# Optimization experiments

Measured on AMD Instinct MI355X. Metric: run time of the kernel, lower is better.

Reference implementation:

```python
import jax, jax.numpy as jnp
import numpy as np

B, S, NB, ORDER, D = 256, 50, 8, 2, 128
N_ITEMS, N_RELS = 100000, 200
STDV = 1.0 / float(np.sqrt(D))  # reset_parameters: uniform(-1/sqrt(hidden), 1/sqrt(hidden))


def setup_inputs() -> dict:
    key = jax.random.key(0)
    ks = jax.random.split(key, 24)
    u = lambda k, shape: jax.random.uniform(k, shape, jnp.float32, -STDV, STDV)
    return {
        'h_iids': jax.random.randint(ks[0], (B, S), 1, N_ITEMS),
        'a_iids': jax.random.randint(ks[1], (B,), 0, N_ITEMS),
        'adj_entity': jax.random.randint(ks[2], (N_ITEMS, NB), 0, N_ITEMS),
        'adj_relation': jax.random.randint(ks[3], (N_ITEMS, NB), 0, N_RELS),
        'item_emb': u(ks[4], (N_ITEMS, D)),
        'rel_emb': u(ks[5], (N_RELS, D)),
        'Wa': u(ks[6], (D, 1)), 'ba': u(ks[7], (1,)),          # linear_attention
        'Wt': u(ks[8], (D, D)), 'bt': u(ks[9], (D,)),          # linear_attention_transform
        'Wih': u(ks[10], (D, 3 * D)), 'Whh': u(ks[11], (D, 3 * D)),  # GRU (1 layer)
        'bih': u(ks[12], (3 * D,)), 'bhh': u(ks[13], (3 * D,)),
        'W1': u(ks[14], (D, D)), 'b1': u(ks[15], (D,)),        # linear_one
        'W2': u(ks[16], (D, D)), 'b2': u(ks[17], (D,)),        # linear_two
        'W3': u(ks[18], (D, 1)),                               # linear_three (no bias)
        'Wtr': u(ks[19], (2 * D, D)), 'btr': u(ks[20], (D,)),  # linear_transform
    }


def _forward(h_iids, adj_entity, adj_relation, item_emb, rel_emb,
             Wa, ba, Wt, bt, Wih, Whh, bih, bhh,
             W1, b1, W2, b2, W3, Wtr, btr):
    # ---- get_neighbors: multi-hop KG neighbor expansion ----
    entities = [h_iids]           # level 0: [B, S]
    relations = []
    for i in range(ORDER):
        e = entities[i]
        entities.append(adj_entity[e].reshape(B, -1))    # [B, S*NB^(i+1)]
        relations.append(adj_relation[e].reshape(B, -1))
    ent_embs = [item_emb[e] for e in entities]           # gathers
    rel_embs = [rel_emb[r] for r in relations]
    # ---- high_order_aggregate: attention-weighted neighbor aggregation ----
    neib = ent_embs[ORDER]                                # [B, S*NB^ORDER, D]
    for i in range(ORDER):
        self_e = ent_embs[ORDER - i - 1]                  # [B, M, D]
        rel = rel_embs[ORDER - i - 1].reshape(B, -1, NB, D)
        nb4 = neib.reshape(rel.shape)                     # [B, M, NB, D]
        att = (self_e[:, :, None, :] * rel * nb4) @ Wa + ba   # [B, M, NB, 1]
        alpha = jax.nn.softmax(att, axis=2)
        agg = jnp.sum(nb4 * alpha, axis=2)                # [B, M, D]
        neib = (self_e + agg) @ Wt + bt                   # aggregate='sum' branch
    item_embs = neib                                      # [B, S, D] (sigmoid in src is dead code)
    # ---- GRU, 1 layer, batch_first ----
    def step(h, x):
        gi = x @ Wih + bih
        gh = h @ Whh + bhh
        ir, iz, inn = jnp.split(gi, 3, axis=-1)
        hr, hz, hn = jnp.split(gh, 3, axis=-1)
        r = jax.nn.sigmoid(ir + hr)
        z = jax.nn.sigmoid(iz + hz)
        n = jnp.tanh(inn + r * hn)
        h2 = (1.0 - z) * n + z * h
        return h2, h2
    h0 = jnp.zeros((B, D), jnp.float32)
    _, outs = jax.lax.scan(step, h0, jnp.swapaxes(item_embs, 0, 1))
    output = jnp.swapaxes(outs, 0, 1)                     # [B, S, D]
    # ---- attention pooling over sequence ----
    last_idx = jnp.clip(jnp.sum(h_iids != 0, axis=1) - 1, 0, S - 1)
    local_ht = output[jnp.arange(B), last_idx]            # [B, D]
    q1 = (local_ht @ W1 + b1)[:, None, :]
    q2 = output @ W2 + b2
    al = jax.nn.sigmoid(q1 + q2) @ W3                     # [B, S, 1]
    global_ht = jnp.sum(al * output, axis=1)
    ght = jnp.concatenate([local_ht, global_ht], axis=1) @ Wtr + btr
    logits = jax.nn.relu(ght @ item_emb.T)                # [B, n_items]
    return logits


def reference(h_iids, a_iids, adj_entity, adj_relation, item_emb, rel_emb,
              Wa, ba, Wt, bt, Wih, Whh, bih, bhh,
              W1, b1, W2, b2, W3, Wtr, btr):
    # a_iids is accepted by forward() but unused (matches the torch source).
    return _forward(h_iids, adj_entity, adj_relation, item_emb, rel_emb,
                    Wa, ba, Wt, bt, Wih, Whh, bih, bhh,
                    W1, b1, W2, b2, W3, Wtr, btr)
```

## Files before the change

### kernel.cpp

```cpp
#include <hip/hip_runtime.h>
#include <hip/hip_bf16.h>
#include <math.h>

#define NB_B 256
#define NB_S 50
#define NB_NB 8
#define NB_D 128
#define NB_NITEMS 100000

#define C_RZ (-1.442695041f)
#define C_N (2.885390082f)

typedef __attribute__((ext_vector_type(8))) short short8;
typedef __attribute__((ext_vector_type(4))) float f32x4;
typedef unsigned int uint;
typedef unsigned short ushort;

__device__ __forceinline__ ushort f2bf(float f) {
  union { float f; uint u; } v;
  v.f = f;
  return (ushort)((v.u + 0x7fffu + ((v.u >> 16) & 1u)) >> 16);
}
__device__ __forceinline__ uint packbf(float a, float b) {
  return (uint)f2bf(a) | ((uint)f2bf(b) << 16);
}
__device__ __forceinline__ float bflo(uint u) {
  union { uint u; float f; } v; v.u = u << 16; return v.f;
}
__device__ __forceinline__ float bfhi(uint u) {
  union { uint u; float f; } v; v.u = u & 0xffff0000u; return v.f;
}
__device__ __forceinline__ float bf2f(ushort u) {
  union { uint u; float f; } v; v.u = (uint)u << 16; return v.f;
}
__device__ __forceinline__ void unpack8(uint4 u, float* f) {
  f[0] = bflo(u.x); f[1] = bfhi(u.x);
  f[2] = bflo(u.y); f[3] = bfhi(u.y);
  f[4] = bflo(u.z); f[5] = bfhi(u.z);
  f[6] = bflo(u.w); f[7] = bfhi(u.w);
}

__device__ __forceinline__ void castf_body(const float* __restrict__ src,
                                           uint* __restrict__ dst, int i, int n8) {
  if (i >= n8) return;
  float4 a = ((const float4*)src)[2 * i];
  float4 b = ((const float4*)src)[2 * i + 1];
  uint4 o;
  o.x = packbf(a.x, a.y);
  o.y = packbf(a.z, a.w);
  o.z = packbf(b.x, b.y);
  o.w = packbf(b.z, b.w);
  ((uint4*)dst)[i] = o;
}
template <int CO, bool SCALED>
__device__ __forceinline__ void castT_body(const float* __restrict__ W,
                                           ushort* __restrict__ WT, int idx) {
  if (idx >= 128 * CO) return;
  int n = idx >> 7, k = idx & 127;
  float v = W[(size_t)k * CO + n];
  if (SCALED) v *= (n < 256 ? C_RZ : C_N);
  WT[idx] = f2bf(v);
}
__global__ __launch_bounds__(256) void prep_kernel(
    const float* __restrict__ item_emb, const float* __restrict__ rel_emb,
    const float* __restrict__ Wt, const float* __restrict__ Wih,
    const float* __restrict__ Whh, const float* __restrict__ W2,
    const float* __restrict__ bih, const float* __restrict__ bhh,
    uint* __restrict__ EMB_BF, uint* __restrict__ REL_BF,
    ushort* __restrict__ WtT, ushort* __restrict__ WihT,
    ushort* __restrict__ WhhT, ushort* __restrict__ W2T,
    float* __restrict__ GIBIAS) {
  int bx = blockIdx.x, tid = threadIdx.x;
  if (bx < 6250) {
    castf_body(item_emb, EMB_BF, bx * 256 + tid, 1600000);
  } else if (bx < 6263) {
    castf_body(rel_emb, REL_BF, (bx - 6250) * 256 + tid, 3200);
  } else if (bx < 6327) {
    castT_body<128, false>(Wt, WtT, (bx - 6263) * 256 + tid);
  } else if (bx < 6519) {
    castT_body<384, true>(Wih, WihT, (bx - 6327) * 256 + tid);
  } else if (bx < 6711) {
    castT_body<384, true>(Whh, WhhT, (bx - 6519) * 256 + tid);
  } else if (bx < 6775) {
    castT_body<128, false>(W2, W2T, (bx - 6711) * 256 + tid);
  } else {
    int idx = (bx - 6775) * 256 + tid;
    if (idx < 384) {
      float s = (idx < 256) ? C_RZ : C_N;
      GIBIAS[idx] = s * bih[idx] + (idx < 256 ? s * bhh[idx] : 0.f);
    }
  }
}

__device__ __forceinline__ uint4 hop_pair4(
    int e_self, int q, int p, const int* __restrict__ adj_e,
    const int* __restrict__ adj_r, const uint* __restrict__ embB,
    const uint* __restrict__ relB, const uint* __restrict__ neibB,
    const float* __restrict__ Wa, float* __restrict__ alds) {
  uint4 us = ((const uint4*)(embB + (size_t)e_self * 64))[q];
  float s[8], wa[8], sw[8];
  unpack8(us, s);
  *(float4*)&wa[0] = ((const float4*)Wa)[q * 2];
  *(float4*)&wa[4] = ((const float4*)Wa)[q * 2 + 1];
#pragma unroll
  for (int d = 0; d < 8; d++) sw[d] = s[d] * wa[d];

  int4 ra = ((const int4*)(adj_r + (size_t)e_self * 8))[0];
  int4 rb = ((const int4*)(adj_r + (size_t)e_self * 8))[1];
  int rk[8] = {ra.x, ra.y, ra.z, ra.w, rb.x, rb.y, rb.z, rb.w};

  uint4 nbp[8];
  if (neibB == nullptr) {
    int4 ea = ((const int4*)(adj_e + (size_t)e_self * 8))[0];
    int4 eb = ((const int4*)(adj_e + (size_t)e_self * 8))[1];
    int e2[8] = {ea.x, ea.y, ea.z, ea.w, eb.x, eb.y, eb.z, eb.w};
#pragma unroll
    for (int k = 0; k < 8; k++)
      nbp[k] = ((const uint4*)(embB + (size_t)e2[k] * 64))[q];
  } else {
#pragma unroll
    for (int k = 0; k < 8; k++)
      nbp[k] = ((const uint4*)(neibB + ((size_t)p * 8 + k) * 64))[q];
  }

  float t[8];
#pragma unroll
  for (int k = 0; k < 8; k++) {
    uint4 ur = ((const uint4*)(relB + (size_t)rk[k] * 64))[q];
    float rr[8], nb[8];
    unpack8(ur, rr);
    unpack8(nbp[k], nb);
    float tt = 0.f;
#pragma unroll
    for (int d = 0; d < 8; d++) tt = fmaf(sw[d] * rr[d], nb[d], tt);
    t[k] = tt;
  }

  bool b0 = (q & 1), b1 = (q & 2), b2 = (q & 4);
  float a4[4];
#pragma unroll
  for (int i = 0; i < 4; i++) {
    float send = b0 ? t[i] : t[4 + i];
    float recv = __shfl_xor(send, 1);
    a4[i] = (b0 ? t[4 + i] : t[i]) + recv;
  }
  float a2[2];
#pragma unroll
  for (int i = 0; i < 2; i++) {
    float send = b1 ? a4[i] : a4[2 + i];
    float recv = __shfl_xor(send, 2);
    a2[i] = (b1 ? a4[2 + i] : a4[i]) + recv;
  }
  float send1 = b2 ? a2[0] : a2[1];
  float recv1 = __shfl_xor(send1, 4);
  float c = (b2 ? a2[1] : a2[0]) + recv1;
  c += __shfl_xor(c, 8);

  float e = __expf(c);
  float den = e;
  den += __shfl_xor(den, 1);
  den += __shfl_xor(den, 2);
  den += __shfl_xor(den, 4);
  float alpha = e * __builtin_amdgcn_rcpf(den);

  int kstar = (q & 1) * 4 + (q & 2) + ((q & 4) >> 2);
  if (q < 8) alds[kstar] = alpha;
  asm volatile("s_waitcnt lgkmcnt(0)" ::: "memory");
  float a8[8];
  *(float4*)&a8[0] = ((const float4*)alds)[0];
  *(float4*)&a8[4] = ((const float4*)alds)[1];

  float x[8];
#pragma unroll
  for (int d = 0; d < 8; d++) x[d] = s[d];
#pragma unroll
  for (int k = 0; k < 8; k++) {
    float nb[8];
    unpack8(nbp[k], nb);
#pragma unroll
    for (int d = 0; d < 8; d++) x[d] = fmaf(a8[k], nb[d], x[d]);
  }
  uint4 o;
  o.x = packbf(x[0], x[1]);
  o.y = packbf(x[2], x[3]);
  o.z = packbf(x[4], x[5]);
  o.w = packbf(x[6], x[7]);
  return o;
}

__global__ __launch_bounds__(256) void hoplin_kernel(
    const int* __restrict__ h_iids, const int* __restrict__ adj_e,
    const int* __restrict__ adj_r, const uint* __restrict__ embB,
    const uint* __restrict__ relB, const float* __restrict__ Wa,
    const ushort* __restrict__ WtT, const float* __restrict__ bt,
    ushort* __restrict__ NEIB) {
  __shared__ ushort X0s[32 * 128];
  __shared__ float als[16][8];
  const int bx = blockIdx.x;
  const int wv = threadIdx.x >> 6, ln = threadIdx.x & 63;
  const int g = ln >> 4, q = ln & 15;
  float* alds = als[wv * 4 + g];

#pragma unroll
  for (int it = 0; it < 2; it++) {
    int lrow = wv * 8 + it * 4 + g;
    int p = bx * 32 + lrow;
    int b = p / (NB_S * NB_NB);
    int m = p % (NB_S * NB_NB);
    int s = m >> 3, jj = m & 7;
    int h = h_iids[b * NB_S + s];
    int e_self = adj_e[h * NB_NB + jj];
    uint4 o = hop_pair4(e_self, q, p, adj_e, adj_r, embB, relB, nullptr, Wa, alds);
    int byte = (lrow * 256 + q * 16) ^ ((lrow & 7) << 4);
    *(uint4*)((char*)X0s + byte) = o;
  }
  __syncthreads();

  const int lr = ln & 15, lg = ln >> 4;
  short8 afr[2][4];
#pragma unroll
  for (int mf = 0; mf < 2; mf++)
#pragma unroll
    for (int kf = 0; kf < 4; kf++) {
      int row = mf * 16 + lr;
      int byte = (row * 256 + lg * 16 + kf * 64) ^ ((row & 7) << 4);
      afr[mf][kf] = *(const short8*)((const char*)X0s + byte);
    }
  f32x4 acc[2][2] = {};
#pragma unroll
  for (int nf = 0; nf < 2; nf++) {
    int n = (wv * 2 + nf) * 16 + lr;
    const ushort* bb = WtT + (size_t)n * 128 + lg * 8;
#pragma unroll
    for (int kf = 0; kf < 4; kf++) {
      short8 b = *(const short8*)(bb + kf * 32);
#pragma unroll
      for (int mf = 0; mf < 2; mf++)
        acc[mf][nf] = __builtin_amdgcn_mfma_f32_16x16x32_bf16(afr[mf][kf], b,
                                                              acc[mf][nf], 0, 0, 0);
    }
  }
#pragma unroll
  for (int mf = 0; mf < 2; mf++)
#pragma unroll
    for (int nf = 0; nf < 2; nf++) {
      int n = (wv * 2 + nf) * 16 + lr;
      float bv = bt[n];
#pragma unroll
      for (int r = 0; r < 4; r++) {
        int mg = bx * 32 + mf * 16 + lg * 4 + r;
        NEIB[(size_t)mg * 128 + n] = f2bf(acc[mf][nf][r] + bv);
      }
    }
}

__global__ __launch_bounds__(256) void hop1_kernel(
    const int* __restrict__ h_iids, const int* __restrict__ adj_e,
    const int* __restrict__ adj_r, const uint* __restrict__ embB,
    const uint* __restrict__ relB, const uint* __restrict__ neibB,
    const float* __restrict__ Wa, uint* __restrict__ Xout) {
  __shared__ float als[16][8];
  const int wv = threadIdx.x >> 6, ln = threadIdx.x & 63;
  const int g = ln >> 4, q = ln & 15;
  int p = blockIdx.x * 16 + wv * 4 + g;
  int e_self = h_iids[p];
  uint4 o = hop_pair4(e_self, q, p, adj_e, adj_r, embB, relB, neibB, Wa,
                      als[wv * 4 + g]);
  ((uint4*)(Xout + (size_t)p * 64))[q] = o;
}

template <int CO, int MPW, bool OUT_BF>
__global__ __launch_bounds__(256) void linm_kernel(
    const ushort* __restrict__ Xbf, const ushort* __restrict__ WT,
    const float* __restrict__ bias, float* __restrict__ Yf,
    ushort* __restrict__ Yb, int nrows) {
  constexpr int NF = CO / 16;
  constexpr int MF = MPW / 16;
  int wave = (int)(blockIdx.x * 4 + (threadIdx.x >> 6));
  int ln = threadIdx.x & 63;
  int m0 = __builtin_amdgcn_readfirstlane(wave) * MPW;
  if (m0 >= nrows) return;
  int lr = ln & 15, lg = ln >> 4;

  short8 afr[MF][4];
#pragma unroll
  for (int mf = 0; mf < MF; mf++) {
    const ushort* ab = Xbf + (size_t)(m0 + mf * 16 + lr) * 128 + lg * 8;
#pragma unroll
    for (int kf = 0; kf < 4; kf++) afr[mf][kf] = *(const short8*)(ab + kf * 32);
  }
  f32x4 acc[MF][NF] = {};
#pragma unroll
  for (int nf = 0; nf < NF; nf++) {
    const ushort* bb = WT + (size_t)(nf * 16 + lr) * 128 + lg * 8;
#pragma unroll
    for (int kf = 0; kf < 4; kf++) {
      short8 b = *(const short8*)(bb + kf * 32);
#pragma unroll
      for (int mf = 0; mf < MF; mf++)
        acc[mf][nf] = __builtin_amdgcn_mfma_f32_16x16x32_bf16(afr[mf][kf], b,
                                                              acc[mf][nf], 0, 0, 0);
    }
  }
#pragma unroll
  for (int mf = 0; mf < MF; mf++)
#pragma unroll
    for (int nf = 0; nf < NF; nf++) {
      int n = nf * 16 + lr;
      float bv = bias[n];
#pragma unroll
      for (int r = 0; r < 4; r++) {
        int m = m0 + mf * 16 + lg * 4 + r;
        float val = acc[mf][nf][r] + bv;
        if (OUT_BF)
          Yb[(size_t)m * CO + n] = f2bf(val);
        else
          Yf[(size_t)m * CO + n] = val;
      }
    }
}

__global__ __launch_bounds__(512) void gru_mfma_kernel(
    const float* __restrict__ GI, const ushort* __restrict__ WhhT_bf,
    const float* __restrict__ bhh, ushort* __restrict__ OUTB) {
  const int b0 = blockIdx.x * 16;
  const int tid = threadIdx.x;
  const int w = tid >> 6, ln = tid & 63;
  const int lr = ln & 15, lg = ln >> 4;
  const int j = w * 16 + lr;

  __shared__ ushort hA[16 * 128];
  __shared__ ushort hB[16 * 128];

  short8 bfr[3][4];
#pragma unroll
  for (int g = 0; g < 3; g++) {
    const ushort* bb = WhhT_bf + (size_t)(g * 128 + j) * 128 + lg * 8;
#pragma unroll
    for (int kf = 0; kf < 4; kf++) bfr[g][kf] = *(const short8*)(bb + kf * 32);
  }
  const float bhn = C_N * bhh[256 + j];

  float h_reg[4] = {0.f, 0.f, 0.f, 0.f};

  {
    uint* hz = (uint*)hA;
#pragma unroll
    for (int i = tid; i < 1024; i += 512) hz[i] = 0;
  }
  __syncthreads();

  float girA[4][3], girB[4][3], girC[4][3], girD[4][3];
#pragma unroll
  for (int r = 0; r < 4; r++) {
    const float* g0 = GI + ((size_t)(b0 + lg * 4 + r) * NB_S + 0) * 384 + j;
    girA[r][0] = g0[0]; girA[r][1] = g0[128]; girA[r][2] = g0[256];
    const float* g1 = GI + ((size_t)(b0 + lg * 4 + r) * NB_S + 1) * 384 + j;
    girB[r][0] = g1[0]; girB[r][1] = g1[128]; girB[r][2] = g1[256];
    const float* g2 = GI + ((size_t)(b0 + lg * 4 + r) * NB_S + 2) * 384 + j;
    girC[r][0] = g2[0]; girC[r][1] = g2[128]; girC[r][2] = g2[256];
  }

  auto STEP = [&](int t, ushort* hRead, ushort* hWrite, float (&cur)[4][3],
                  float (&pre3)[4][3]) {
    if (t + 3 < NB_S) {
#pragma unroll
      for (int r = 0; r < 4; r++) {
        const float* g = GI + ((size_t)(b0 + lg * 4 + r) * NB_S + (t + 3)) * 384 + j;
        pre3[r][0] = g[0]; pre3[r][1] = g[128]; pre3[r][2] = g[256];
      }
    }
    __builtin_amdgcn_sched_barrier(0);
    short8 afr[4];
#pragma unroll
    for (int kf = 0; kf < 4; kf++) {
      int byte = (lr * 256 + kf * 64 + lg * 16) ^ ((lr & 7) << 4);
      afr[kf] = *(const short8*)((const char*)hRead + byte);
    }
    f32x4 acc[3] = {};
#pragma unroll
    for (int g = 0; g < 3; g++)
#pragma unroll
      for (int kf = 0; kf < 4; kf++)
        acc[g] = __builtin_amdgcn_mfma_f32_16x16x32_bf16(afr[kf], bfr[g][kf],
                                                         acc[g], 0, 0, 0);
#pragma unroll
    for (int r = 0; r < 4; r++) {
      int b = lg * 4 + r;
      float rg = __builtin_amdgcn_rcpf(
          1.f + __builtin_amdgcn_exp2f(cur[r][0] + acc[0][r]));
      float ze = __builtin_amdgcn_exp2f(cur[r][1] + acc[1][r]);
      float xp = cur[r][2] + rg * (bhn + acc[2][r]);
      float e2 = __builtin_amdgcn_exp2f(xp);
      float n = 1.f - 2.f * __builtin_amdgcn_rcpf(e2 + 1.f);
      float h2 = n + (h_reg[r] - n) * __builtin_amdgcn_rcpf(1.f + ze);
      h_reg[r] = h2;
      ushort hb = f2bf(h2);
      OUTB[((size_t)(b0 + b) * NB_S + t) * 128 + j] = hb;
      int byte = (b * 256 + j * 2) ^ ((b & 7) << 4);
      *(ushort*)((char*)hWrite + byte) = hb;
    }
    asm volatile("s_waitcnt lgkmcnt(0)" ::: "memory");
    __builtin_amdgcn_s_barrier();
  };

  for (int g4 = 0; g4 < 12; g4++) {
    int t = g4 * 4;
    STEP(t + 0, hA, hB, girA, girD);
    STEP(t + 1, hB, hA, girB, girA);
    STEP(t + 2, hA, hB, girC, girB);
    STEP(t + 3, hB, hA, girD, girC);
  }
  STEP(48, hA, hB, girA, girD);
  STEP(49, hB, hA, girB, girA);
}

__global__ __launch_bounds__(256) void pool_kernel(
    const int* __restrict__ h_iids, const ushort* __restrict__ OUTB,
    const float* __restrict__ W1, const float* __restrict__ b1,
    const ushort* __restrict__ W2T, const float* __restrict__ b2,
    const float* __restrict__ W3, const float* __restrict__ Wtr,
    const float* __restrict__ btr, ushort* __restrict__ GHT_bf) {
  const int b = blockIdx.x, tid = threadIdx.x;
  __shared__ float lh[128];
  __shared__ float q1[128];
  __shared__ float al[64];
  __shared__ float cat[256];

  if (tid < 128) {
    int cnt = 0;
    for (int s = 0; s < NB_S; s++) cnt += (h_iids[b * NB_S + s] != 0);
    int li = min(max(cnt - 1, 0), NB_S - 1);
    lh[tid] = bf2f(OUTB[((size_t)b * NB_S + li) * 128 + tid]);
  }
  __syncthreads();
  if (tid < 128) {
    float acc = b1[tid];
    for (int d = 0; d < 128; d++) acc += lh[d] * W1[(size_t)d * 128 + tid];
    q1[tid] = acc;
  }
  __syncthreads();

  {
    const int wv = tid >> 6, ln = tid & 63, lr = ln & 15, lg = ln >> 4;
    const int s0 = wv * 16;
    short8 zz = {0, 0, 0, 0, 0, 0, 0, 0};
    short8 afr[4];
    int srow = s0 + lr;
#pragma unroll
    for (int kf = 0; kf < 4; kf++)
      afr[kf] = (srow < NB_S)
                    ? *(const short8*)(OUTB + ((size_t)b * NB_S + srow) * 128 +
                                       lg * 8 + kf * 32)
                    : zz;
    float part[4] = {0.f, 0.f, 0.f, 0.f};
#pragma unroll
    for (int nf = 0; nf < 8; nf++) {
      const ushort* bb = W2T + (size_t)(nf * 16 + lr) * 128 + lg * 8;
      f32x4 acc = {};
#pragma unroll
      for (int kf = 0; kf < 4; kf++) {
        short8 bv = *(const short8*)(bb + kf * 32);
        acc = __builtin_amdgcn_mfma_f32_16x16x32_bf16(afr[kf], bv, acc, 0, 0, 0);
      }
      int c = nf * 16 + lr;
      float qc = q1[c] + b2[c];
      float w3 = W3[c];
#pragma unroll
      for (int r = 0; r < 4; r++)
        part[r] += w3 / (1.f + __expf(-(qc + acc[r])));
    }
#pragma unroll
    for (int r = 0; r < 4; r++) {
#pragma unroll
      for (int off = 1; off < 16; off <<= 1) part[r] += __shfl_xor(part[r], off);
      int s = s0 + lg * 4 + r;
      if (lr == 0 && s < NB_S) al[s] = part[r];
    }
  }
  __syncthreads();

  if (tid < 128) {
    float g = 0.f;
    for (int s = 0; s < NB_S; s++)
      g += al[s] * bf2f(OUTB[((size_t)b * NB_S + s) * 128 + tid]);
    cat[tid] = lh[tid];
    cat[128 + tid] = g;
  }
  __syncthreads();
  if (tid < 128) {
    float acc = btr[tid];
    for (int dd = 0; dd < 256; dd++) acc += cat[dd] * Wtr[(size_t)dd * 128 + tid];
    GHT_bf[b * 128 + tid] = f2bf(acc);
  }
}

__global__ __launch_bounds__(256) void logits_mfma_kernel(
    const ushort* __restrict__ GHT_bf, const ushort* __restrict__ embB,
    float* __restrict__ out) {
  int wave = (int)(blockIdx.x * 4 + (threadIdx.x >> 6));
  int ln = threadIdx.x & 63;
  int n0 = __builtin_amdgcn_readfirstlane(wave) * 32;
  if (n0 >= NB_NITEMS) return;
  int lr = ln & 15, lg = ln >> 4;

  short8 bfr[2][4];
#pragma unroll
  for (int nf = 0; nf < 2; nf++) {
    const ushort* base = embB + (size_t)(n0 + nf * 16 + lr) * 128 + lg * 8;
#pragma unroll
    for (int kf = 0; kf < 4; kf++) bfr[nf][kf] = *(const short8*)(base + kf * 32);
  }

  f32x4 acc[16][2] = {};
#pragma unroll
  for (int mg = 0; mg < 4; mg++) {
    short8 afr[4][4];
#pragma unroll
    for (int mf = 0; mf < 4; mf++) {
      const ushort* ab = GHT_bf + (size_t)((mg * 4 + mf) * 16 + lr) * 128 + lg * 8;
#pragma unroll
      for (int kf = 0; kf < 4; kf++) afr[mf][kf] = *(const short8*)(ab + kf * 32);
    }
#pragma unroll
    for (int mf = 0; mf < 4; mf++)
#pragma unroll
      for (int nf = 0; nf < 2; nf++)
#pragma unroll
        for (int kf = 0; kf < 4; kf++)
          acc[mg * 4 + mf][nf] = __builtin_amdgcn_mfma_f32_16x16x32_bf16(
              afr[mf][kf], bfr[nf][kf], acc[mg * 4 + mf][nf], 0, 0, 0);
  }

#pragma unroll
  for (int mf = 0; mf < 16; mf++)
#pragma unroll
    for (int nf = 0; nf < 2; nf++) {
      int n = n0 + nf * 16 + lr;
#pragma unroll
      for (int r = 0; r < 4; r++) {
        int m = mf * 16 + lg * 4 + r;
        out[(size_t)m * NB_NITEMS + n] = fmaxf(acc[mf][nf][r], 0.f);
      }
    }
}

extern "C" void kernel_launch(void* const* d_in, const int* in_sizes, int n_in,
                              void* d_out, int out_size, void* d_ws, size_t ws_size,
                              hipStream_t stream) {
  const int* h_iids = (const int*)d_in[0];
  const int* adj_e = (const int*)d_in[2];
  const int* adj_r = (const int*)d_in[3];
  const float* item_emb = (const float*)d_in[4];
  const float* rel_emb = (const float*)d_in[5];
  const float* Wa = (const float*)d_in[6];
  const float* Wt = (const float*)d_in[8];
  const float* bt = (const float*)d_in[9];
  const float* Wih = (const float*)d_in[10];
  const float* Whh = (const float*)d_in[11];
  const float* bih = (const float*)d_in[12];
  const float* bhh = (const float*)d_in[13];
  const float* W1 = (const float*)d_in[14];
  const float* b1 = (const float*)d_in[15];
  const float* W2 = (const float*)d_in[16];
  const float* b2 = (const float*)d_in[17];
  const float* W3 = (const float*)d_in[18];
  const float* Wtr = (const float*)d_in[19];
  const float* btr = (const float*)d_in[20];
  float* out = (float*)d_out;

  char* w = (char*)d_ws;
  uint* EMB_BF = (uint*)w;                    w += 25600000;
  uint* REL_BF = (uint*)w;                    w += 51200;
  ushort* WtT_bf = (ushort*)w;                w += 32768;
  ushort* WihT_bf = (ushort*)w;               w += 98304;
  ushort* WhhT_bf = (ushort*)w;               w += 98304;
  ushort* W2T_bf = (ushort*)w;                w += 32768;
  float* GIBIAS = (float*)w;                  w += 2048;
  uint* NEIB_bf = (uint*)w;                   w += 26214400;
  uint* X1_bf = (uint*)w;                     w += 3276800;
  uint* SEQ_bf = (uint*)w;                    w += 3276800;
  float* GI = (float*)w;                      w += 19660800;
  ushort* GHT_bf = (ushort*)w;                w += 65536;

  ushort* OUTB = (ushort*)X1_bf;

  prep_kernel<<<6777, 256, 0, stream>>>(item_emb, rel_emb, Wt, Wih, Whh, W2,
                                        bih, bhh, EMB_BF, REL_BF, WtT_bf,
                                        WihT_bf, WhhT_bf, W2T_bf, GIBIAS);

  hoplin_kernel<<<3200, 256, 0, stream>>>(h_iids, adj_e, adj_r, EMB_BF, REL_BF,
                                          Wa, WtT_bf, bt, (ushort*)NEIB_bf);
  hop1_kernel<<<800, 256, 0, stream>>>(h_iids, adj_e, adj_r, EMB_BF, REL_BF,
                                       NEIB_bf, Wa, X1_bf);
  linm_kernel<128, 32, true><<<100, 256, 0, stream>>>(
      (const ushort*)X1_bf, WtT_bf, bt, nullptr, (ushort*)SEQ_bf, 12800);
  linm_kernel<384, 16, false><<<200, 256, 0, stream>>>(
      (const ushort*)SEQ_bf, WihT_bf, GIBIAS, GI, nullptr, 12800);

  gru_mfma_kernel<<<16, 512, 0, stream>>>(GI, WhhT_bf, bhh, OUTB);
  pool_kernel<<<256, 256, 0, stream>>>(h_iids, OUTB, W1, b1, W2T_bf, b2, W3,
                                       Wtr, btr, GHT_bf);

  logits_mfma_kernel<<<782, 256, 0, stream>>>(GHT_bf, (const ushort*)EMB_BF, out);
}
```

Before: 226.9 us.

## Fuse hop-1 aggregation with Wt transform and GRU input projection

```diff
diff --git a/kernel.cpp b/kernel.cpp
--- a/kernel.cpp
+++ b/kernel.cpp
@@ -254,70 +254,88 @@
     }
 }
 
-__global__ __launch_bounds__(256) void hop1_kernel(
+__global__ __launch_bounds__(256) void hopgi_kernel(
     const int* __restrict__ h_iids, const int* __restrict__ adj_e,
     const int* __restrict__ adj_r, const uint* __restrict__ embB,
     const uint* __restrict__ relB, const uint* __restrict__ neibB,
-    const float* __restrict__ Wa, uint* __restrict__ Xout) {
+    const float* __restrict__ Wa, const ushort* __restrict__ WtT,
+    const float* __restrict__ bt, const ushort* __restrict__ WihT,
+    const float* __restrict__ GIBIAS, float* __restrict__ GI) {
+  __shared__ ushort X1s[16 * 128];
+  __shared__ ushort SEQs[16 * 128];
   __shared__ float als[16][8];
   const int wv = threadIdx.x >> 6, ln = threadIdx.x & 63;
   const int g = ln >> 4, q = ln & 15;
-  int p = blockIdx.x * 16 + wv * 4 + g;
+  const int lp = wv * 4 + g;
+  const int p = blockIdx.x * 16 + lp;
+
   int e_self = h_iids[p];
-  uint4 o = hop_pair4(e_self, q, p, adj_e, adj_r, embB, relB, neibB, Wa,
-                      als[wv * 4 + g]);
-  ((uint4*)(Xout + (size_t)p * 64))[q] = o;
-}
-
-template <int CO, int MPW, bool OUT_BF>
-__global__ __launch_bounds__(256) void linm_kernel(
-    const ushort* __restrict__ Xbf, const ushort* __restrict__ WT,
-    const float* __restrict__ bias, float* __restrict__ Yf,
-    ushort* __restrict__ Yb, int nrows) {
-  constexpr int NF = CO / 16;
-  constexpr int MF = MPW / 16;
-  int wave = (int)(blockIdx.x * 4 + (threadIdx.x >> 6));
-  int ln = threadIdx.x & 63;
-  int m0 = __builtin_amdgcn_readfirstlane(wave) * MPW;
-  if (m0 >= nrows) return;
-  int lr = ln & 15, lg = ln >> 4;
-
-  short8 afr[MF][4];
-#pragma unroll
-  for (int mf = 0; mf < MF; mf++) {
-    const ushort* ab = Xbf + (size_t)(m0 + mf * 16 + lr) * 128 + lg * 8;
-#pragma unroll
-    for (int kf = 0; kf < 4; kf++) afr[mf][kf] = *(const short8*)(ab + kf * 32);
-  }
-  f32x4 acc[MF][NF] = {};
-#pragma unroll
-  for (int nf = 0; nf < NF; nf++) {
-    const ushort* bb = WT + (size_t)(nf * 16 + lr) * 128 + lg * 8;
+  uint4 o = hop_pair4(e_self, q, p, adj_e, adj_r, embB, relB, neibB, Wa, als[lp]);
+  {
+    int byte = (lp * 256 + q * 16) ^ ((lp & 7) << 4);
+    *(uint4*)((char*)X1s + byte) = o;
+  }
+  __syncthreads();
+
+  const int lr = ln & 15, lg = ln >> 4;
+  {
+    short8 afr[4];
 #pragma unroll
     for (int kf = 0; kf < 4; kf++) {
-      short8 b = *(const short8*)(bb + kf * 32);
-#pragma unroll
-      for (int mf = 0; mf < MF; mf++)
-        acc[mf][nf] = __builtin_amdgcn_mfma_f32_16x16x32_bf16(afr[mf][kf], b,
-                                                              acc[mf][nf], 0, 0, 0);
-    }
-  }
-#pragma unroll
-  for (int mf = 0; mf < MF; mf++)
-#pragma unroll
-    for (int nf = 0; nf < NF; nf++) {
-      int n = nf * 16 + lr;
-      float bv = bias[n];
+      int byte = (lr * 256 + lg * 16 + kf * 64) ^ ((lr & 7) << 4);
+      afr[kf] = *(const short8*)((const char*)X1s + byte);
+    }
+    f32x4 acc[2] = {};
+#pragma unroll
+    for (int nf = 0; nf < 2; nf++) {
+      int n = (wv * 2 + nf) * 16 + lr;
+      const ushort* bb = WtT + (size_t)n * 128 + lg * 8;
+#pragma unroll
+      for (int kf = 0; kf < 4; kf++) {
+        short8 b = *(const short8*)(bb + kf * 32);
+        acc[nf] = __builtin_amdgcn_mfma_f32_16x16x32_bf16(afr[kf], b, acc[nf],
+                                                          0, 0, 0);
+      }
+    }
+#pragma unroll
+    for (int nf = 0; nf < 2; nf++) {
+      int n = (wv * 2 + nf) * 16 + lr;
+      float bv = bt[n];
 #pragma unroll
       for (int r = 0; r < 4; r++) {
-        int m = m0 + mf * 16 + lg * 4 + r;
-        float val = acc[mf][nf][r] + bv;
-        if (OUT_BF)
-          Yb[(size_t)m * CO + n] = f2bf(val);
-        else
-          Yf[(size_t)m * CO + n] = val;
-      }
-    }
+        int m = lg * 4 + r;
+        int byte = (m * 256 + n * 2) ^ ((m & 7) << 4);
+        *(ushort*)((char*)SEQs + byte) = f2bf(acc[nf][r] + bv);
+      }
+    }
+  }
+  __syncthreads();
+
+  {
+    short8 sfr[4];
+#pragma unroll
+    for (int kf = 0; kf < 4; kf++) {
+      int byte = (lr * 256 + lg * 16 + kf * 64) ^ ((lr & 7) << 4);
+      sfr[kf] = *(const short8*)((const char*)SEQs + byte);
+    }
+#pragma unroll
+    for (int i = 0; i < 6; i++) {
+      int n = (wv * 6 + i) * 16 + lr;
+      const ushort* bb = WihT + (size_t)n * 128 + lg * 8;
+      f32x4 a2 = {};
+#pragma unroll
+      for (int kf = 0; kf < 4; kf++) {
+        short8 b = *(const short8*)(bb + kf * 32);
+        a2 = __builtin_amdgcn_mfma_f32_16x16x32_bf16(sfr[kf], b, a2, 0, 0, 0);
+      }
+      float bv = GIBIAS[n];
+#pragma unroll
+      for (int r = 0; r < 4; r++) {
+        int m = lg * 4 + r;
+        GI[(size_t)(blockIdx.x * 16 + m) * 384 + n] = a2[r] + bv;
+      }
+    }
+  }
 }
 
 __global__ __launch_bounds__(512) void gru_mfma_kernel(
@@ -578,12 +596,9 @@
   ushort* W2T_bf = (ushort*)w;                w += 32768;
   float* GIBIAS = (float*)w;                  w += 2048;
   uint* NEIB_bf = (uint*)w;                   w += 26214400;
-  uint* X1_bf = (uint*)w;                     w += 3276800;
-  uint* SEQ_bf = (uint*)w;                    w += 3276800;
   float* GI = (float*)w;                      w += 19660800;
+  ushort* OUTB = (ushort*)w;                  w += 3276800;
   ushort* GHT_bf = (ushort*)w;                w += 65536;
-
-  ushort* OUTB = (ushort*)X1_bf;
 
   prep_kernel<<<6777, 256, 0, stream>>>(item_emb, rel_emb, Wt, Wih, Whh, W2,
                                         bih, bhh, EMB_BF, REL_BF, WtT_bf,
@@ -591,12 +606,9 @@
 
   hoplin_kernel<<<3200, 256, 0, stream>>>(h_iids, adj_e, adj_r, EMB_BF, REL_BF,
                                           Wa, WtT_bf, bt, (ushort*)NEIB_bf);
-  hop1_kernel<<<800, 256, 0, stream>>>(h_iids, adj_e, adj_r, EMB_BF, REL_BF,
-                                       NEIB_bf, Wa, X1_bf);
-  linm_kernel<128, 32, true><<<100, 256, 0, stream>>>(
-      (const ushort*)X1_bf, WtT_bf, bt, nullptr, (ushort*)SEQ_bf, 12800);
-  linm_kernel<384, 16, false><<<200, 256, 0, stream>>>(
-      (const ushort*)SEQ_bf, WihT_bf, GIBIAS, GI, nullptr, 12800);
+  hopgi_kernel<<<800, 256, 0, stream>>>(h_iids, adj_e, adj_r, EMB_BF, REL_BF,
+                                        NEIB_bf, Wa, WtT_bf, bt, WihT_bf,
+                                        GIBIAS, GI);
 
   gru_mfma_kernel<<<16, 512, 0, stream>>>(GI, WhhT_bf, bhh, OUTB);
   pool_kernel<<<256, 256, 0, stream>>>(h_iids, OUTB, W1, b1, W2T_bf, b2, W3,
```

After: 215.3 us. 1.05x faster.
